# Optimization experiments

Hardware: AMD Instinct MI355X
Metric: run time of the kernel (lower is better)

## Reference

```python
import jax, jax.numpy as jnp
import numpy as np

B, S, HID = 4, 2048, 1024
H, D = 16, 64  # num_attention_heads, attention_head_size


def setup_inputs() -> dict:
    key = jax.random.key(0)
    k1, k2, k3, k4 = jax.random.split(key, 4)
    scale = 0.02
    return {
        "hidden_states": jax.random.normal(k1, (B, S, HID), dtype=jnp.float32),
        "attention_mask": jnp.zeros((B, 1, 1, S), dtype=jnp.float32),
        "Wq": jax.random.normal(k2, (HID, HID), dtype=jnp.float32) * scale,
        "bq": jnp.zeros((HID,), dtype=jnp.float32),
        "Wk": jax.random.normal(k3, (HID, HID), dtype=jnp.float32) * scale,
        "bk": jnp.zeros((HID,), dtype=jnp.float32),
        "Wv": jax.random.normal(k4, (HID, HID), dtype=jnp.float32) * scale,
        "bv": jnp.zeros((HID,), dtype=jnp.float32),
    }


def _split_heads(x):
    # [B,S,HID] -> [B,H,S,D]
    b, s, _ = x.shape
    return x.reshape(b, s, H, D).transpose(0, 2, 1, 3)


def reference(hidden_states, attention_mask, Wq, bq, Wk, bk, Wv, bv):
    # nn.Linear applies x @ W.T + b
    q = _split_heads(hidden_states @ Wq.T + bq)  # [B,H,S,D]
    k = _split_heads(hidden_states @ Wk.T + bk)
    v = _split_heads(hidden_states @ Wv.T + bv)
    scores = jnp.einsum("bhqd,bhkd->bhqk", q, k) / jnp.sqrt(jnp.float32(D))
    scores = scores + attention_mask  # additive mask, broadcast [B,1,1,S]
    probs = jax.nn.softmax(scores, axis=-1)  # dropout prob = 0 -> identity
    ctx = jnp.einsum("bhqk,bhkd->bhqd", probs, v)  # [B,H,S,D]
    ctx = ctx.transpose(0, 2, 1, 3).reshape(hidden_states.shape[0], hidden_states.shape[1], HID)
    return ctx
```

## Files before the change

### kernel.cpp

```cpp
#include <hip/hip_runtime.h>
#include <stdint.h>

#define BB 4
#define SS 2048
#define HID 1024
#define NH 16
#define DH 64

using bf16x8 = __attribute__((ext_vector_type(8))) short;
using f32x4  = __attribute__((ext_vector_type(4))) float;

#define LOG2E 1.44269504088896340736f

__device__ __forceinline__ ushort f2bf(float f) {
  union { float f; uint32_t u; } v; v.f = f;
  return (ushort)((v.u + 0x7FFFu + ((v.u >> 16) & 1u)) >> 16);
}

__device__ __forceinline__ uint32_t cvt_pk_bf16(float a, float b) {
  uint32_t r;
  asm("v_cvt_pk_bf16_f32 %0, %1, %2" : "=v"(r) : "v"(a), "v"(b));
  return r;
}

__device__ __forceinline__ float exp2_hw(float x) {
  float r;
  asm("v_exp_f32 %0, %1" : "=v"(r) : "v"(x));
  return r;
}

__device__ __forceinline__ void gload_lds16(const ushort* g, ushort* l) {
  __builtin_amdgcn_global_load_lds(
      (const __attribute__((address_space(1))) uint32_t*)g,
      (__attribute__((address_space(3))) uint32_t*)l, 16, 0, 0);
}

__device__ __forceinline__ int vperm(int j) {
  return (j & 0x23) | ((j & 0x0C) << 1) | ((j & 0x10) >> 2);
}

__global__ void cvt_kernel(const float* __restrict__ x, const float* __restrict__ wq,
                           const float* __restrict__ wk, const float* __restrict__ wv,
                           const float* __restrict__ am,
                           ushort* __restrict__ xbf, ushort* __restrict__ wbf,
                           float* __restrict__ maskL) {
  const int64_t NX4 = (int64_t)BB * SS * HID / 4;
  const int64_t NW4 = (int64_t)HID * HID / 4;
  const int64_t NWT = 3 * NW4;
  int64_t i = (int64_t)blockIdx.x * blockDim.x + threadIdx.x;
  if (i >= NX4 + NWT) {
    const int64_t jm = i - (NX4 + NWT);
    float4 v = ((const float4*)am)[jm];
    v.x *= LOG2E; v.y *= LOG2E; v.z *= LOG2E; v.w *= LOG2E;
    ((float4*)maskL)[jm] = v;
    return;
  }
  float4 v;
  ushort4* dst;
  if (i < NX4) {
    v = ((const float4*)x)[i];
    dst = (ushort4*)xbf + i;
  } else {
    int64_t j = i - NX4;
    int w = (int)(j >> 18);
    int64_t k = j & (NW4 - 1);
    const float* src = (w == 0) ? wq : (w == 1) ? wk : wv;
    v = ((const float4*)src)[k];
    dst = (ushort4*)wbf + j;
  }
  ushort4 o;
  o.x = f2bf(v.x); o.y = f2bf(v.y); o.z = f2bf(v.z); o.w = f2bf(v.w);
  *dst = o;
}

__global__ __launch_bounds__(512, 2) void qkv_gemm(
    const ushort* __restrict__ xbf, const ushort* __restrict__ wbf,
    const float* __restrict__ bq, const float* __restrict__ bk,
    const float* __restrict__ bv,
    ushort* __restrict__ qws, ushort* __restrict__ kws, ushort* __restrict__ vtws) {
  __shared__ short Al[2][256][64];
  __shared__ short Bl[2][192][64];

  const int tid = threadIdx.x, wid = tid >> 6, lane = tid & 63;
  const int colL = lane & 15, rowg = lane >> 4;
  const int wr = wid >> 2, wc = wid & 3;

  const int wgid = (blockIdx.x & 7) * 64 + (blockIdx.x >> 3);
  const int m0 = (wgid >> 4) * 256;
  const int n0 = (wgid & 15) * 192;

  const int swzcol = (((tid & 7) * 16) ^ (((tid >> 3) & 7) << 4)) >> 1;
  const ushort* aSrc = xbf + (int64_t)(m0 + (tid >> 3)) * HID + swzcol;
  const ushort* bSrc = wbf + (int64_t)(n0 + (tid >> 3)) * HID + swzcol;
  ushort* Al_u = (ushort*)&Al[0][0][0];
  ushort* Bl_u = (ushort*)&Bl[0][0][0];

  auto stageA = [&](int kt, int r, int ps) {
    gload_lds16(aSrc + r * 64 * HID + kt * 64, Al_u + ps * 16384 + r * 4096 + wid * 512);
  };
  auto stageB = [&](int kt, int r, int ps) {
    gload_lds16(bSrc + r * 64 * HID + kt * 64, Bl_u + ps * 12288 + r * 4096 + wid * 512);
  };

  const int xsw = (colL & 7) << 4;
  const int offk0 = (rowg * 16) ^ xsw;
  const int offk1 = (64 + rowg * 16) ^ xsw;
  const int arow = (wr * 128 + colL) * 128;
  const int brow = (wc * 48 + colL) * 128;
  const char* AlC = (const char*)&Al[0][0][0];
  const char* BlC = (const char*)&Bl[0][0][0];

  f32x4 acc[8][3];
#pragma unroll
  for (int i = 0; i < 8; ++i)
#pragma unroll
    for (int j = 0; j < 3; ++j)
#pragma unroll
      for (int r = 0; r < 4; ++r) acc[i][j][r] = 0.f;

  stageB(0, 0, 0); stageB(0, 1, 0); stageB(0, 2, 0);
  stageA(0, 0, 0); stageA(0, 2, 0); stageA(0, 1, 0); stageA(0, 3, 0);
  asm volatile("s_waitcnt vmcnt(2)" ::: "memory");
  __builtin_amdgcn_s_barrier();

#define DO_PHASE(P, S1, S2, PRE_BAR2)                                          \
  {                                                                            \
    const int mfa = 2 * (P), mfb = 2 * (P) + 1;                                \
    bf16x8 aA0 = *(const bf16x8*)(kA0 + mfa * 2048);                           \
    bf16x8 aA1 = *(const bf16x8*)(kA1 + mfa * 2048);                           \
    bf16x8 aB0 = *(const bf16x8*)(kA0 + mfb * 2048);                           \
    bf16x8 aB1 = *(const bf16x8*)(kA1 + mfb * 2048);                           \
    S1; S2;                                                                    \
    __builtin_amdgcn_s_barrier();                                              \
    __builtin_amdgcn_s_setprio(1);                                             \
    _Pragma("unroll")                                                          \
    for (int nf = 0; nf < 3; ++nf) {                                           \
      acc[mfa][nf] = __builtin_amdgcn_mfma_f32_16x16x32_bf16(aA0, bfr[nf][0], acc[mfa][nf], 0, 0, 0); \
      acc[mfa][nf] = __builtin_amdgcn_mfma_f32_16x16x32_bf16(aA1, bfr[nf][1], acc[mfa][nf], 0, 0, 0); \
      acc[mfb][nf] = __builtin_amdgcn_mfma_f32_16x16x32_bf16(aB0, bfr[nf][0], acc[mfb][nf], 0, 0, 0); \
      acc[mfb][nf] = __builtin_amdgcn_mfma_f32_16x16x32_bf16(aB1, bfr[nf][1], acc[mfb][nf], 0, 0, 0); \
    }                                                                          \
    __builtin_amdgcn_s_setprio(0);                                             \
    PRE_BAR2;                                                                  \
    __builtin_amdgcn_s_barrier();                                              \
  }

  for (int t = 0; t < 16; ++t) {
    const int p = t & 1;
    const int ps = p ^ 1;
    const bool st = (t < 15);
    const int kt = t + 1;
    const char* kA0 = AlC + p * 32768 + arow + offk0;
    const char* kA1 = AlC + p * 32768 + arow + offk1;
    const char* kB0 = BlC + p * 24576 + brow + offk0;
    const char* kB1 = BlC + p * 24576 + brow + offk1;

    bf16x8 bfr[3][2];
#pragma unroll
    for (int nf = 0; nf < 3; ++nf) {
      bfr[nf][0] = *(const bf16x8*)(kB0 + nf * 2048);
      bfr[nf][1] = *(const bf16x8*)(kB1 + nf * 2048);
    }

    DO_PHASE(0, if (st) stageB(kt, 0, ps), if (st) stageB(kt, 1, ps), )
    DO_PHASE(1, if (st) stageB(kt, 2, ps), if (st) stageA(kt, 0, ps),
             if (t == 15) { asm volatile("s_waitcnt vmcnt(0)" ::: "memory"); }
             else        { asm volatile("s_waitcnt vmcnt(4)" ::: "memory"); })
    DO_PHASE(2, if (st) stageA(kt, 2, ps), if (st) stageA(kt, 1, ps), )
    DO_PHASE(3, if (st) stageA(kt, 3, ps), ,
             if (t == 14) { asm volatile("s_waitcnt vmcnt(0)" ::: "memory"); }
             else if (st) { asm volatile("s_waitcnt vmcnt(2)" ::: "memory"); })
  }
#undef DO_PHASE

#pragma unroll
  for (int nf = 0; nf < 3; ++nf) {
    const int n = n0 + wc * 48 + nf * 16 + colL;
    const int which = n >> 10;
    const int c = n & 1023;
    const int h = c >> 6, d = c & 63;
    const float bias = ((which == 0) ? bq : (which == 1) ? bk : bv)[c];
#pragma unroll
    for (int mf = 0; mf < 8; ++mf) {
      const int mb = m0 + wr * 128 + mf * 16 + rowg * 4;
      const int b = mb >> 11, s = mb & 2047;
      const int bh = b * NH + h;
      if (which == 2) {
        ushort4 o;
        o.x = f2bf(acc[mf][nf][0] + bias);
        o.y = f2bf(acc[mf][nf][1] + bias);
        o.z = f2bf(acc[mf][nf][2] + bias);
        o.w = f2bf(acc[mf][nf][3] + bias);
        const int scol2 = (s & ~63) | vperm(s & 63);
        *(ushort4*)&vtws[((int64_t)bh * DH + d) * SS + scol2] = o;
      } else {
        ushort* dst = (which == 0) ? qws : kws;
#pragma unroll
        for (int r = 0; r < 4; ++r)
          dst[((int64_t)bh * SS + s + r) * DH + d] = f2bf(acc[mf][nf][r] + bias);
      }
    }
  }
}

__global__ __launch_bounds__(256, 4) void attn_kernel(
    const ushort* __restrict__ qws, const ushort* __restrict__ kws,
    const ushort* __restrict__ vtws, const float* __restrict__ maskL,
    float* __restrict__ out) {
  __shared__ short Kl[2][64][64];
  __shared__ short Vl[2][64][64];

  const int tid = threadIdx.x, wid = tid >> 6, lane = tid & 63;
  const int bh = blockIdx.x, qb = blockIdx.y;
  const int b = bh >> 4, h = bh & 15;
  const int64_t qkb = (int64_t)bh * SS * DH;
  const int64_t vb  = (int64_t)bh * DH * SS;
  const int q0 = qb * 128;
  const int colL = lane & 15, rowg = lane >> 4;
  const float SCL = 0.125f * LOG2E;

  const int srow = wid * 16 + (lane >> 3);
  const int swzc = (((lane & 7) * 16) ^ ((lane >> 3) << 4)) >> 1;
  const ushort* gk = kws + qkb + (int64_t)srow * DH + swzc;
  const ushort* gv = vtws + vb + (int64_t)srow * SS + swzc;
  ushort* ldsK = (ushort*)&Kl[0][0][0] + wid * 1024;
  ushort* ldsV = (ushort*)&Vl[0][0][0] + wid * 1024;

  auto stageKV = [&](int bufsel, int tt) {
    const ushort* k0 = gk + tt * 4096;
    gload_lds16(k0,       ldsK + bufsel * 4096);
    gload_lds16(k0 + 512, ldsK + bufsel * 4096 + 512);
    const ushort* v0 = gv + tt * 64;
    gload_lds16(v0,          ldsV + bufsel * 4096);
    gload_lds16(v0 + 8 * SS, ldsV + bufsel * 4096 + 512);
  };

  const int xsw = (colL & 7) << 4;
  const char* kb0 = (const char*)&Kl[0][0][0] + colL * 128 + ((rowg * 16) ^ xsw);
  const char* kb1 = (const char*)&Kl[0][0][0] + colL * 128 + ((64 + rowg * 16) ^ xsw);
  const char* vb0 = (const char*)&Vl[0][0][0] + colL * 128 + ((rowg * 16) ^ xsw);
  const char* vb1 = (const char*)&Vl[0][0][0] + colL * 128 + ((64 + rowg * 16) ^ xsw);

  bf16x8 qf[2][2];
#pragma unroll
  for (int qh = 0; qh < 2; ++qh) {
    const ushort* gq = qws + qkb + (int64_t)(q0 + wid * 32 + qh * 16 + colL) * DH + rowg * 8;
    qf[qh][0] = *(const bf16x8*)(gq);
    qf[qh][1] = *(const bf16x8*)(gq + 32);
  }

  const f32x4 FZERO = {0.f, 0.f, 0.f, 0.f};
  union OU { uint32_t u[4]; bf16x8 v; } onesu;
  onesu.u[0] = 0x3F803F80u; onesu.u[1] = 0x3F803F80u;
  onesu.u[2] = 0x3F803F80u; onesu.u[3] = 0x3F803F80u;
  const bf16x8 ONES = onesu.v;

  f32x4 accO[2][4];
  f32x4 accL[2];
#pragma unroll
  for (int qh = 0; qh < 2; ++qh) {
    accL[qh] = FZERO;
#pragma unroll
    for (int dt = 0; dt < 4; ++dt)
#pragma unroll
      for (int r = 0; r < 4; ++r) accO[qh][dt][r] = 0.f;
  }

  const float* mrow = maskL + b * SS + rowg * 4;

  stageKV(0, 0);
  __syncthreads();

  auto step = [&](int t, int bufc) {
    if (t + 1 < SS / 64) stageKV(bufc ^ 1, t + 1);

    f32x4 sc[2][4];
    __builtin_amdgcn_s_setprio(1);
#pragma unroll
    for (int kt = 0; kt < 4; ++kt) {
      bf16x8 kf0 = *(const bf16x8*)(kb0 + bufc * 8192 + kt * 2048);
      bf16x8 kf1 = *(const bf16x8*)(kb1 + bufc * 8192 + kt * 2048);
      sc[0][kt] = __builtin_amdgcn_mfma_f32_16x16x32_bf16(kf0, qf[0][0], FZERO, 0, 0, 0);
      sc[0][kt] = __builtin_amdgcn_mfma_f32_16x16x32_bf16(kf1, qf[0][1], sc[0][kt], 0, 0, 0);
      sc[1][kt] = __builtin_amdgcn_mfma_f32_16x16x32_bf16(kf0, qf[1][0], FZERO, 0, 0, 0);
      sc[1][kt] = __builtin_amdgcn_mfma_f32_16x16x32_bf16(kf1, qf[1][1], sc[1][kt], 0, 0, 0);
    }
    __builtin_amdgcn_s_setprio(0);

    float4 m4[4];
#pragma unroll
    for (int kt = 0; kt < 4; ++kt)
      m4[kt] = *(const float4*)(mrow + t * 64 + kt * 16);

    bf16x8 paf[2][2];
#pragma unroll
    for (int qh = 0; qh < 2; ++qh) {
#pragma unroll
      for (int kt = 0; kt < 4; ++kt) {
        sc[qh][kt][0] = exp2_hw(fmaf(sc[qh][kt][0], SCL, m4[kt].x));
        sc[qh][kt][1] = exp2_hw(fmaf(sc[qh][kt][1], SCL, m4[kt].y));
        sc[qh][kt][2] = exp2_hw(fmaf(sc[qh][kt][2], SCL, m4[kt].z));
        sc[qh][kt][3] = exp2_hw(fmaf(sc[qh][kt][3], SCL, m4[kt].w));
      }
      union PU { uint32_t u[4]; bf16x8 v; } p0, p1;
      p0.u[0] = cvt_pk_bf16(sc[qh][0][0], sc[qh][0][1]);
      p0.u[1] = cvt_pk_bf16(sc[qh][0][2], sc[qh][0][3]);
      p0.u[2] = cvt_pk_bf16(sc[qh][1][0], sc[qh][1][1]);
      p0.u[3] = cvt_pk_bf16(sc[qh][1][2], sc[qh][1][3]);
      p1.u[0] = cvt_pk_bf16(sc[qh][2][0], sc[qh][2][1]);
      p1.u[1] = cvt_pk_bf16(sc[qh][2][2], sc[qh][2][3]);
      p1.u[2] = cvt_pk_bf16(sc[qh][3][0], sc[qh][3][1]);
      p1.u[3] = cvt_pk_bf16(sc[qh][3][2], sc[qh][3][3]);
      paf[qh][0] = p0.v;
      paf[qh][1] = p1.v;
    }

    __builtin_amdgcn_s_setprio(1);
#pragma unroll
    for (int ks = 0; ks < 2; ++ks) {
      accL[0] = __builtin_amdgcn_mfma_f32_16x16x32_bf16(paf[0][ks], ONES, accL[0], 0, 0, 0);
      accL[1] = __builtin_amdgcn_mfma_f32_16x16x32_bf16(paf[1][ks], ONES, accL[1], 0, 0, 0);
#pragma unroll
      for (int dt = 0; dt < 4; ++dt) {
        bf16x8 vf = *(const bf16x8*)((ks == 0 ? vb0 : vb1) + bufc * 8192 + dt * 2048);
        accO[0][dt] = __builtin_amdgcn_mfma_f32_16x16x32_bf16(paf[0][ks], vf, accO[0][dt], 0, 0, 0);
        accO[1][dt] = __builtin_amdgcn_mfma_f32_16x16x32_bf16(paf[1][ks], vf, accO[1][dt], 0, 0, 0);
      }
    }
    __builtin_amdgcn_s_setprio(0);
    __syncthreads();
  };

  for (int t = 0; t < SS / 64; t += 2) {
    step(t, 0);
    step(t + 1, 1);
  }

#pragma unroll
  for (int qh = 0; qh < 2; ++qh) {
    float inv[4];
#pragma unroll
    for (int r = 0; r < 4; ++r) inv[r] = 1.0f / accL[qh][r];
#pragma unroll
    for (int dt = 0; dt < 4; ++dt)
#pragma unroll
      for (int r = 0; r < 4; ++r) {
        const int s = q0 + wid * 32 + qh * 16 + rowg * 4 + r;
        out[((int64_t)b * SS + s) * HID + h * DH + dt * 16 + colL] = accO[qh][dt][r] * inv[r];
      }
  }
}

extern "C" void kernel_launch(void* const* d_in, const int* in_sizes, int n_in,
                              void* d_out, int out_size, void* d_ws, size_t ws_size,
                              hipStream_t stream) {
  const float* x  = (const float*)d_in[0];
  const float* am = (const float*)d_in[1];
  const float* wq = (const float*)d_in[2];
  const float* bq = (const float*)d_in[3];
  const float* wk = (const float*)d_in[4];
  const float* bk = (const float*)d_in[5];
  const float* wv = (const float*)d_in[6];
  const float* bv = (const float*)d_in[7];
  float* out = (float*)d_out;
  char* ws = (char*)d_ws;

  ushort* xbf  = (ushort*)(ws);
  ushort* wbf  = (ushort*)(ws + 16777216);
  ushort* qws  = (ushort*)(ws + 23068672);
  ushort* kws  = (ushort*)(ws + 39845888);
  ushort* vtws = (ushort*)(ws + 56623104);
  float*  mskL = (float*)(ws + 73400320);

  hipLaunchKernelGGL(cvt_kernel, dim3(11272), dim3(256), 0, stream,
                     x, wq, wk, wv, am, xbf, wbf, mskL);
  hipLaunchKernelGGL(qkv_gemm, dim3(512), dim3(512), 0, stream,
                     xbf, wbf, bq, bk, bv, qws, kws, vtws);
  hipLaunchKernelGGL(attn_kernel, dim3(64, 16), dim3(256), 0, stream,
                     qws, kws, vtws, mskL, out);
}
```

Baseline: 154.6 us.

## Software-pipeline QK and PV across KV tiles with split K/V staging and LDS mask

Restructures the attention main loop so the QK^T MFMAs for tile t overlap the softmax and PV of tile t-1, using two score register sets. K and V staging are issued at different points with explicit vmcnt waits and raw s_barrier instead of __syncthreads. The additive mask row is preloaded once into LDS rather than read from global memory each step. Occupancy hint drops from 4 to 3 blocks per CU to accommodate the extra registers and LDS, which may reduce latency hiding.

```diff
diff --git a/kernel.cpp b/kernel.cpp
--- a/kernel.cpp
+++ b/kernel.cpp
@@ -203,12 +203,13 @@
   }
 }
 
-__global__ __launch_bounds__(256, 4) void attn_kernel(
+__global__ __launch_bounds__(256, 3) void attn_kernel(
     const ushort* __restrict__ qws, const ushort* __restrict__ kws,
     const ushort* __restrict__ vtws, const float* __restrict__ maskL,
     float* __restrict__ out) {
   __shared__ short Kl[2][64][64];
   __shared__ short Vl[2][64][64];
+  __shared__ float Ml[2048];
 
   const int tid = threadIdx.x, wid = tid >> 6, lane = tid & 63;
   const int bh = blockIdx.x, qb = blockIdx.y;
@@ -226,13 +227,20 @@
   ushort* ldsK = (ushort*)&Kl[0][0][0] + wid * 1024;
   ushort* ldsV = (ushort*)&Vl[0][0][0] + wid * 1024;
 
-  auto stageKV = [&](int bufsel, int tt) {
+  auto stageK = [&](int slot, int tt) {
     const ushort* k0 = gk + tt * 4096;
-    gload_lds16(k0,       ldsK + bufsel * 4096);
-    gload_lds16(k0 + 512, ldsK + bufsel * 4096 + 512);
+    gload_lds16(k0,       ldsK + slot * 4096);
+    gload_lds16(k0 + 512, ldsK + slot * 4096 + 512);
+  };
+  auto stageV = [&](int slot, int tt) {
     const ushort* v0 = gv + tt * 64;
-    gload_lds16(v0,          ldsV + bufsel * 4096);
-    gload_lds16(v0 + 8 * SS, ldsV + bufsel * 4096 + 512);
+    gload_lds16(v0,          ldsV + slot * 4096);
+    gload_lds16(v0 + 8 * SS, ldsV + slot * 4096 + 512);
+  };
+  auto stageMask = [&]() {
+    const float* src = maskL + b * SS + (wid * 2) * 256 + lane * 4;
+    gload_lds16((const ushort*)src,         (ushort*)(Ml + wid * 2 * 256));
+    gload_lds16((const ushort*)(src + 256), (ushort*)(Ml + wid * 2 * 256 + 256));
   };
 
   const int xsw = (colL & 7) << 4;
@@ -266,33 +274,28 @@
       for (int r = 0; r < 4; ++r) accO[qh][dt][r] = 0.f;
   }
 
-  const float* mrow = maskL + b * SS + rowg * 4;
-
-  stageKV(0, 0);
-  __syncthreads();
-
-  auto step = [&](int t, int bufc) {
-    if (t + 1 < SS / 64) stageKV(bufc ^ 1, t + 1);
-
-    f32x4 sc[2][4];
+  f32x4 scA[2][4], scB[2][4];
+  bf16x8 paf[2][2];
+
+  auto qk = [&](int cur, f32x4 (&sc)[2][4]) {
     __builtin_amdgcn_s_setprio(1);
 #pragma unroll
     for (int kt = 0; kt < 4; ++kt) {
-      bf16x8 kf0 = *(const bf16x8*)(kb0 + bufc * 8192 + kt * 2048);
-      bf16x8 kf1 = *(const bf16x8*)(kb1 + bufc * 8192 + kt * 2048);
+      bf16x8 kf0 = *(const bf16x8*)(kb0 + cur * 8192 + kt * 2048);
+      bf16x8 kf1 = *(const bf16x8*)(kb1 + cur * 8192 + kt * 2048);
       sc[0][kt] = __builtin_amdgcn_mfma_f32_16x16x32_bf16(kf0, qf[0][0], FZERO, 0, 0, 0);
       sc[0][kt] = __builtin_amdgcn_mfma_f32_16x16x32_bf16(kf1, qf[0][1], sc[0][kt], 0, 0, 0);
       sc[1][kt] = __builtin_amdgcn_mfma_f32_16x16x32_bf16(kf0, qf[1][0], FZERO, 0, 0, 0);
       sc[1][kt] = __builtin_amdgcn_mfma_f32_16x16x32_bf16(kf1, qf[1][1], sc[1][kt], 0, 0, 0);
     }
     __builtin_amdgcn_s_setprio(0);
-
+  };
+
+  auto soft = [&](int tm, f32x4 (&sc)[2][4]) {
     float4 m4[4];
 #pragma unroll
     for (int kt = 0; kt < 4; ++kt)
-      m4[kt] = *(const float4*)(mrow + t * 64 + kt * 16);
-
-    bf16x8 paf[2][2];
+      m4[kt] = *(const float4*)&Ml[tm * 64 + kt * 16 + rowg * 4];
 #pragma unroll
     for (int qh = 0; qh < 2; ++qh) {
 #pragma unroll
@@ -314,7 +317,9 @@
       paf[qh][0] = p0.v;
       paf[qh][1] = p1.v;
     }
-
+  };
+
+  auto pv = [&](int slot) {
     __builtin_amdgcn_s_setprio(1);
 #pragma unroll
     for (int ks = 0; ks < 2; ++ks) {
@@ -322,19 +327,53 @@
       accL[1] = __builtin_amdgcn_mfma_f32_16x16x32_bf16(paf[1][ks], ONES, accL[1], 0, 0, 0);
 #pragma unroll
       for (int dt = 0; dt < 4; ++dt) {
-        bf16x8 vf = *(const bf16x8*)((ks == 0 ? vb0 : vb1) + bufc * 8192 + dt * 2048);
+        bf16x8 vf = *(const bf16x8*)((ks == 0 ? vb0 : vb1) + slot * 8192 + dt * 2048);
         accO[0][dt] = __builtin_amdgcn_mfma_f32_16x16x32_bf16(paf[0][ks], vf, accO[0][dt], 0, 0, 0);
         accO[1][dt] = __builtin_amdgcn_mfma_f32_16x16x32_bf16(paf[1][ks], vf, accO[1][dt], 0, 0, 0);
       }
     }
     __builtin_amdgcn_s_setprio(0);
-    __syncthreads();
-  };
-
-  for (int t = 0; t < SS / 64; t += 2) {
-    step(t, 0);
-    step(t + 1, 1);
-  }
+  };
+
+  auto fullstep = [&](int t, f32x4 (&scN)[2][4], f32x4 (&scO)[2][4],
+                      bool stg, bool dopv) {
+    const int cur = t & 1, prv = cur ^ 1;
+    if (stg) stageK(prv, t + 1);
+    qk(cur, scN);
+    if (dopv) {
+      soft(t - 1, scO);
+      pv(prv);
+    }
+    __builtin_amdgcn_sched_barrier(0);
+    __builtin_amdgcn_s_barrier();
+    __builtin_amdgcn_sched_barrier(0);
+    if (stg) {
+      stageV(prv, t + 1);
+      __builtin_amdgcn_sched_barrier(0);
+      asm volatile("s_waitcnt vmcnt(2)" ::: "memory");
+    } else {
+      asm volatile("s_waitcnt vmcnt(0)" ::: "memory");
+    }
+    __builtin_amdgcn_s_barrier();
+    __builtin_amdgcn_sched_barrier(0);
+  };
+
+  stageMask();
+  stageK(0, 0);
+  stageV(0, 0);
+  asm volatile("s_waitcnt vmcnt(2)" ::: "memory");
+  __builtin_amdgcn_s_barrier();
+  __builtin_amdgcn_sched_barrier(0);
+
+  fullstep(0, scA, scB, true, false);
+  for (int t = 1; t < 31; t += 2) {
+    fullstep(t,     scB, scA, true, true);
+    fullstep(t + 1, scA, scB, true, true);
+  }
+  fullstep(31, scB, scA, false, true);
+
+  soft(31, scB);
+  pv(1);
 
 #pragma unroll
   for (int qh = 0; qh < 2; ++qh) {
```

Measured after the change: 160.5 us. +3.8%, slower.
